# Kernel tuning notes

Hardware: AMD Instinct MI355X
Metric: run time of the kernel (lower is better)

The kernel has to match this reference:

```python
import jax, jax.numpy as jnp
import numpy as np

H, B, T = 4, 16, 4000
E, D, A, C, K, O = 512, 512, 128, 10, 101, 512


def setup_inputs() -> dict:
    key = jax.random.key(0)
    ks = jax.random.split(key, 12)
    return {
        "enc_pad": jax.random.normal(ks[0], (B, T, E), jnp.float32),
        "enc_len": jax.random.randint(ks[1], (B,), T // 2, T + 1, jnp.int32),
        "dec_z": jax.random.normal(ks[2], (B, D), jnp.float32),
        "att_prev": jax.random.uniform(ks[3], (H, B, T), jnp.float32) / T,
        # learned parameters (per-head stacks)
        "Wenc": jax.random.normal(ks[4], (H, E, A), jnp.float32) / np.sqrt(E).astype(np.float32),
        "benc": jnp.zeros((H, A), jnp.float32),
        "Wdec": jax.random.normal(ks[5], (H, D, A), jnp.float32) / np.sqrt(D).astype(np.float32),
        "Watt": jax.random.normal(ks[6], (H, C, A), jnp.float32) / np.sqrt(C).astype(np.float32),
        "conv_w": jax.random.normal(ks[7], (H, C, K), jnp.float32) / np.sqrt(K).astype(np.float32),
        "gv": jax.random.normal(ks[8], (H, A), jnp.float32) / np.sqrt(A).astype(np.float32),
        "Wo": jax.random.normal(ks[9], (H * E, O), jnp.float32) / np.sqrt(H * E).astype(np.float32),
        "bo": jnp.zeros((O,), jnp.float32),
    }


def reference(enc_pad, enc_len, dec_z, att_prev, Wenc, benc, Wdec, Watt, conv_w, gv, Wo, bo):
    scaling = 1.0
    Hh, Bb, Tt = att_prev.shape
    Cc, Kk = conv_w.shape[1], conv_w.shape[2]
    pad_l = Kk // 2
    pad_r = Kk // 2 if Kk % 2 == 1 else Kk // 2 - 1
    # location conv: grouped 1D conv over heads. lhs [B,H,Tp], rhs [H*C,1,K]
    x = jnp.pad(att_prev.transpose(1, 0, 2), ((0, 0), (0, 0), (pad_l, pad_r)))
    rhs = conv_w.reshape(Hh * Cc, 1, Kk)
    conv = jax.lax.conv_general_dilated(
        x, rhs, window_strides=(1,), padding='VALID',
        dimension_numbers=('NCH', 'OIH', 'NCH'), feature_group_count=Hh)  # [B,H*C,T]
    conv = conv.reshape(Bb, Hh, Cc, Tt)
    att_conv = jnp.einsum('bhct,hca->bhta', conv, Watt)                    # mlp_att
    enc_proj = jnp.einsum('bte,hea->bhta', enc_pad, Wenc) + benc[None, :, None, :]  # mlp_enc
    dec_proj = jnp.einsum('bd,hda->bha', dec_z, Wdec)[:, :, None, :]       # mlp_dec
    e = jnp.einsum('bhta,ha->bht', jnp.tanh(enc_proj + dec_proj + att_conv), gv)  # gvec
    w = jax.nn.softmax(scaling * e, axis=-1)                               # [B,H,T]
    c = jnp.einsum('bht,bte->bhe', w, enc_pad).reshape(Bb, Hh * enc_pad.shape[-1])
    out = c @ Wo + bo                                                      # mlp_o
    return out, w.transpose(1, 0, 2)  # ws stacked as [H,B,T]
```

## Files before the change

### kernel.cpp

```cpp
#include <hip/hip_runtime.h>
#include <hip/hip_bf16.h>

#define H_ 4
#define B_ 16
#define T_ 4000
#define E_ 512
#define D_ 512
#define A_ 128
#define C_ 10
#define K_ 101
#define O_ 512
#define TC_ 50
#define CH_ (T_ / TC_)

typedef __attribute__((ext_vector_type(4))) float f32x4;
typedef __attribute__((ext_vector_type(8)))  short short8;

#define MFMA16(a, b, c) __builtin_amdgcn_mfma_f32_16x16x32_bf16(a, b, c, 0, 0, 0)

#define GLL16(gp, lp) __builtin_amdgcn_global_load_lds( \
    (const __attribute__((address_space(1))) unsigned int*)(gp), \
    (__attribute__((address_space(3))) unsigned int*)(lp), 16, 0, 0)

static __device__ __forceinline__ unsigned short f2bf(float x) {
  unsigned u = __float_as_uint(x);
  unsigned r = (u + 0x7FFFu + ((u >> 16) & 1u)) >> 16;
  return (unsigned short)r;
}
static __device__ __forceinline__ unsigned pk2(float a, float b) {
  return (unsigned)f2bf(a) | ((unsigned)f2bf(b) << 16);
}
static __device__ __forceinline__ unsigned cvtpk(float lo, float hi) {
  unsigned r;
  asm("v_cvt_pk_bf16_f32 %0, %1, %2" : "=v"(r) : "v"(lo), "v"(hi));
  return r;
}
static __device__ __forceinline__ uint4 packbf8(float4 f0, float4 f1) {
  uint4 u;
  u.x = cvtpk(f0.x, f0.y); u.y = cvtpk(f0.z, f0.w);
  u.z = cvtpk(f1.x, f1.y); u.w = cvtpk(f1.z, f1.w);
  return u;
}
static __device__ __forceinline__ float tanh_fast(float x) {
  return 1.0f - 2.0f / (__expf(2.0f * x) + 1.0f);
}
static __device__ __forceinline__ int swz(int r) {
  return (r & 3) ^ ((r >> 2) & 3);
}

__global__ __launch_bounds__(256) void k_prep(const float* __restrict__ Wenc,
                                              const float* __restrict__ Watt,
                                              const float* __restrict__ dec_z,
                                              const float* __restrict__ Wdec,
                                              const float* __restrict__ benc,
                                              char* __restrict__ wbs2,
                                              char* __restrict__ wattb2,
                                              float* __restrict__ addv4) {
  const int bid = blockIdx.x;
  const int tid = threadIdx.x;
  if (bid < 128) {
    const int c = bid * 256 + tid;
    const int kt = c >> 11;
    const int ci = c & 2047;
    const int col = ci >> 2, cc = ci & 3;
    const int h = col >> 7, a = col & 127;
    const int kk = kt * 32 + ((cc ^ swz(col)) & 3) * 8;
    const float* w = Wenc + ((size_t)h * E_ + kk) * A_ + a;
    uint4 u;
    u.x = pk2(w[0], w[A_]);
    u.y = pk2(w[2 * A_], w[3 * A_]);
    u.z = pk2(w[4 * A_], w[5 * A_]);
    u.w = pk2(w[6 * A_], w[7 * A_]);
    ((uint4*)wbs2)[c] = u;
  } else if (bid == 128) {
#pragma unroll
    for (int q = 0; q < 4; ++q) {
      const int cw = q * 256 + tid;
      const int h = cw >> 8;
      const int rr = cw & 255;
      const int col = rr >> 1, half = rr & 1;
      unsigned short v[8];
#pragma unroll
      for (int j = 0; j < 8; ++j) {
        const int k = half * 8 + j;
        v[j] = (k < C_) ? f2bf(Watt[((size_t)h * C_ + k) * A_ + col]) : (unsigned short)0;
      }
      uint4 u;
      u.x = (unsigned)v[0] | ((unsigned)v[1] << 16);
      u.y = (unsigned)v[2] | ((unsigned)v[3] << 16);
      u.z = (unsigned)v[4] | ((unsigned)v[5] << 16);
      u.w = (unsigned)v[6] | ((unsigned)v[7] << 16);
      ((uint4*)wattb2)[cw] = u;
    }
  } else {
    const int idx = bid - 129;
    const int b = idx >> 3, h = (idx >> 1) & 3, ks = idx & 1;
    const int a = tid & 127, kh = tid >> 7;
    const int p = ks * 2 + kh;
    const int d0 = p * 128;
    const float* z = dec_z + (size_t)b * D_ + d0;
    const float* w = Wdec + ((size_t)h * D_ + d0) * A_ + a;
    float s = (p == 0) ? benc[h * A_ + a] : 0.f;
#pragma unroll 8
    for (int d = 0; d < 128; ++d) s += z[d] * w[(size_t)d * A_];
    addv4[(((size_t)p * B_ + b) * H_ + h) * A_ + a] = s;
  }
}

__global__ __launch_bounds__(256) void k_conv(const float* __restrict__ att_prev,
                                              const float* __restrict__ conv_w,
                                              char* __restrict__ convpad) {
  const int bh = blockIdx.x;
  const int b = bh / H_, h = bh % H_;
  const int t0 = blockIdx.y * 256;
  __shared__ float ap[256 + K_ - 1 + 3];
  __shared__ float cw[C_ * K_];
  const float* src = att_prev + ((size_t)h * B_ + b) * T_;
  for (int i = threadIdx.x; i < 256 + K_ - 1; i += 256) {
    int tt = t0 - (K_ / 2) + i;
    ap[i] = (tt >= 0 && tt < T_) ? src[tt] : 0.f;
  }
  for (int i = threadIdx.x; i < C_ * K_; i += 256) cw[i] = conv_w[(size_t)h * C_ * K_ + i];
  __syncthreads();
  const int t = t0 + threadIdx.x;
  if (t < T_) {
    float s[C_];
#pragma unroll
    for (int c = 0; c < C_; ++c) s[c] = 0.f;
    for (int k = 0; k < K_; ++k) {
      float apv = ap[threadIdx.x + k];
#pragma unroll
      for (int c = 0; c < C_; ++c) s[c] += cw[c * K_ + k] * apv;
    }
    uint4 u0, u1;
    u0.x = pk2(s[0], s[1]); u0.y = pk2(s[2], s[3]);
    u0.z = pk2(s[4], s[5]); u0.w = pk2(s[6], s[7]);
    u1.x = pk2(s[8], s[9]); u1.y = 0u; u1.z = 0u; u1.w = 0u;
    char* dst = convpad + (size_t)(b * T_ + t) * 128 + h * 32;
    *(uint4*)dst = u0;
    *(uint4*)(dst + 16) = u1;
  }
}

__global__ __launch_bounds__(512, 4) void k_fused_e_mfma(
    const float* __restrict__ enc,
    const char*  __restrict__ wbs2,
    const char*  __restrict__ convpad,
    const char*  __restrict__ wattb2,
    const float* __restrict__ addv4,
    const float* __restrict__ gv,
    float* __restrict__ e_out) {
  __shared__ char smem[73728];
  const int tid = threadIdx.x;
  const int wv = tid >> 6;
  const int lane = tid & 63, l15 = lane & 15, lg = lane >> 4;
  const int m0 = blockIdx.x * 64;
  const int h = wv >> 1;
  const bool aRole = (wv < 4);

  f32x4 acc[4][4];
#pragma unroll
  for (int i = 0; i < 4; ++i)
#pragma unroll
    for (int j = 0; j < 4; ++j) acc[i][j] = (f32x4){0.f, 0.f, 0.f, 0.f};

  int aOff[4], bOff[4];
#pragma unroll
  for (int q = 0; q < 4; ++q) {
    const int row = q * 16 + l15;
    aOff[q] = row * 64 + (((lg ^ swz(row)) & 3) << 4);
    const int col = wv * 64 + q * 16 + l15;
    bOff[q] = col * 64 + (((lg ^ swz(col)) & 3) << 4);
  }

  const int arow = tid >> 2, ac = tid & 3;
  const int ks = ((ac ^ swz(arow)) & 3) * 8;
  const float* eR = enc + (size_t)(m0 + arow) * E_ + ks;
  const int wOff = arow * 64 + ac * 16;
  const char* bsrc = wbs2 + (size_t)(wv - 4) * 8192 + lane * 16;
  char* bdstBase = smem + 8192 + (wv - 4) * 8192;

  float4 X0, X1;
  const float* eP = eR + 64;
  const char* bsP = bsrc + 32768;

  if (aRole) {
    float4 c0 = *(const float4*)eR;
    float4 c1 = *(const float4*)(eR + 4);
    X0 = *(const float4*)(eR + 32);
    X1 = *(const float4*)(eR + 36);
    *(uint4*)(smem + wOff) = packbf8(c0, c1);
    asm volatile("s_waitcnt vmcnt(2) lgkmcnt(0)" ::: "memory");
  } else {
#pragma unroll
    for (int i = 0; i < 8; ++i)
      GLL16(bsrc + i * 1024, bdstBase + i * 1024);
    asm volatile("s_waitcnt vmcnt(0) lgkmcnt(0)" ::: "memory");
  }
  __builtin_amdgcn_sched_barrier(0);
  __builtin_amdgcn_s_barrier();

#pragma unroll 1
  for (int kt = 0; kt < 16; ++kt) {
    const int cur = kt & 1;
    const char* bufA = smem + cur * 4096;
    const char* bufB = smem + 8192 + cur * 32768;

    if (!aRole && kt < 15) {
      char* d = smem + 8192 + (cur ^ 1) * 32768 + (wv - 4) * 8192;
#pragma unroll
      for (int i = 0; i < 8; ++i)
        GLL16(bsP + i * 1024, d + i * 1024);
    }
    __builtin_amdgcn_sched_barrier(0);

    short8 aF[4];
#pragma unroll
    for (int q = 0; q < 4; ++q) aF[q] = *(const short8*)(bufA + aOff[q]);
    __builtin_amdgcn_s_setprio(1);
#pragma unroll
    for (int qn = 0; qn < 4; ++qn) {
      short8 bF = *(const short8*)(bufB + bOff[qn]);
#pragma unroll
      for (int qm = 0; qm < 4; ++qm)
        acc[qm][qn] = MFMA16(aF[qm], bF, acc[qm][qn]);
    }
    __builtin_amdgcn_s_setprio(0);

    if (aRole) {
      if (kt < 15)
        *(uint4*)(smem + (cur ^ 1) * 4096 + wOff) = packbf8(X0, X1);
      if (kt < 14) {
        X0 = *(const float4*)eP;
        X1 = *(const float4*)(eP + 4);
        eP += 32;
      }
    } else {
      bsP += 32768;
    }

    if (kt < 14) {
      if (aRole)
        asm volatile("s_waitcnt vmcnt(2) lgkmcnt(0)" ::: "memory");
      else
        asm volatile("s_waitcnt vmcnt(0) lgkmcnt(0)" ::: "memory");
    } else {
      asm volatile("s_waitcnt vmcnt(0) lgkmcnt(0)" ::: "memory");
    }
    __builtin_amdgcn_sched_barrier(0);
    __builtin_amdgcn_s_barrier();
  }

  {
    short8 zf;
#pragma unroll
    for (int i = 0; i < 8; ++i) zf[i] = 0;
    short8 cf[4], wf[4];
#pragma unroll
    for (int q = 0; q < 4; ++q) { cf[q] = zf; wf[q] = zf; }
    if (lg < 2) {
#pragma unroll
      for (int q = 0; q < 4; ++q) {
        const int row = m0 + q * 16 + l15;
        cf[q] = *(const short8*)(convpad + (size_t)row * 128 + h * 32 + lg * 16);
        const int col = (wv & 1) * 64 + q * 16 + l15;
        wf[q] = *(const short8*)(wattb2 + ((size_t)h * 128 + col) * 32 + lg * 16);
      }
    }
#pragma unroll
    for (int qm = 0; qm < 4; ++qm)
#pragma unroll
      for (int qn = 0; qn < 4; ++qn)
        acc[qm][qn] = MFMA16(cf[qm], wf[qn], acc[qm][qn]);
  }

  {
    const unsigned b0w = (unsigned)m0 / 4000u;
    const unsigned b1w = (unsigned)(m0 + 63) / 4000u;
    float av0[4], av1[4], gvr[4];
#pragma unroll
    for (int qn = 0; qn < 4; ++qn) {
      const int col = (wv & 1) * 64 + qn * 16 + l15;
      const int i0 = (int)b0w * 512 + h * 128 + col;
      const int i1 = (int)b1w * 512 + h * 128 + col;
      av0[qn] = addv4[i0] + addv4[8192 + i0] + addv4[16384 + i0] + addv4[24576 + i0];
      av1[qn] = addv4[i1] + addv4[8192 + i1] + addv4[16384 + i1] + addv4[24576 + i1];
      gvr[qn] = gv[h * 128 + col];
    }
    float* Pb = (float*)smem;
#pragma unroll
    for (int qm = 0; qm < 4; ++qm) {
#pragma unroll
      for (int r = 0; r < 4; ++r) {
        const int rowLocal = qm * 16 + lg * 4 + r;
        const unsigned brow = (unsigned)(m0 + rowLocal);
        const unsigned bb = brow / 4000u;
        const int sel = (bb != b0w);
        float s = 0.f;
#pragma unroll
        for (int qn = 0; qn < 4; ++qn)
          s += gvr[qn] * tanh_fast(acc[qm][qn][r] + (sel ? av1[qn] : av0[qn]));
        s += __shfl_xor(s, 1);
        s += __shfl_xor(s, 2);
        s += __shfl_xor(s, 4);
        s += __shfl_xor(s, 8);
        if (l15 == 0) Pb[wv * 64 + rowLocal] = s;
      }
    }
  }
  __syncthreads();
  if (tid < 256) {
    const float* Pb = (const float*)smem;
    const int hh = tid >> 6, r = tid & 63;
    const float ev = Pb[(hh * 2) * 64 + r] + Pb[(hh * 2 + 1) * 64 + r];
    const unsigned brow = (unsigned)(m0 + r);
    const unsigned bb = brow / 4000u;
    const unsigned tt = brow - bb * 4000u;
    e_out[((size_t)bb * H_ + hh) * T_ + tt] = ev;
  }
}

__global__ __launch_bounds__(256) void k_msum(const float* __restrict__ e_in,
                                              float2* __restrict__ msum) {
  const int bh = blockIdx.x;
  const float* er = e_in + (size_t)bh * T_;
  __shared__ float red[256];
  const int tid = threadIdx.x;
  float m = -1e30f;
  for (int t = tid; t < T_; t += 256) m = fmaxf(m, er[t]);
  red[tid] = m;
  __syncthreads();
  for (int s = 128; s > 0; s >>= 1) {
    if (tid < s) red[tid] = fmaxf(red[tid], red[tid + s]);
    __syncthreads();
  }
  m = red[0];
  __syncthreads();
  float sum = 0.f;
  for (int t = tid; t < T_; t += 256) sum += __expf(er[t] - m);
  red[tid] = sum;
  __syncthreads();
  for (int s = 128; s > 0; s >>= 1) {
    if (tid < s) red[tid] += red[tid + s];
    __syncthreads();
  }
  if (tid == 0) msum[bh] = make_float2(m, 1.0f / red[0]);
}

__global__ __launch_bounds__(512) void k_ctx(const float* __restrict__ enc,
                                             const float* __restrict__ e_in,
                                             const float2* __restrict__ msum,
                                             float* __restrict__ wout,
                                             float* __restrict__ partial) {
  const int b = blockIdx.x, tc = blockIdx.y;
  const int t0 = tc * CH_;
  const int tid = threadIdx.x;
  const int grp = tid >> 7, lt = tid & 127;
  __shared__ float wls[H_ * CH_];
  __shared__ float4 red[3][4][128];
  for (int i = tid; i < H_ * CH_; i += 512) {
    const int h = i / CH_, tt = i - h * CH_;
    const float2 ms = msum[b * H_ + h];
    const float w = __expf(e_in[((size_t)b * H_ + h) * T_ + t0 + tt] - ms.x) * ms.y;
    wls[i] = w;
    wout[((size_t)h * B_ + b) * T_ + t0 + tt] = w;
  }
  __syncthreads();
  float4 a0 = {0,0,0,0}, a1 = {0,0,0,0}, a2 = {0,0,0,0}, a3 = {0,0,0,0};
  const float4* enc4 = (const float4*)enc;
  const int tg = grp * 20;
  const size_t ebase = ((size_t)b * T_ + t0 + tg) * 128 + lt;
#pragma unroll 5
  for (int tt = 0; tt < 20; ++tt) {
    const float4 x = enc4[ebase + (size_t)tt * 128];
    const float w0 = wls[tg + tt];
    const float w1 = wls[CH_ + tg + tt];
    const float w2 = wls[2 * CH_ + tg + tt];
    const float w3 = wls[3 * CH_ + tg + tt];
    a0.x += w0 * x.x; a0.y += w0 * x.y; a0.z += w0 * x.z; a0.w += w0 * x.w;
    a1.x += w1 * x.x; a1.y += w1 * x.y; a1.z += w1 * x.z; a1.w += w1 * x.w;
    a2.x += w2 * x.x; a2.y += w2 * x.y; a2.z += w2 * x.z; a2.w += w2 * x.w;
    a3.x += w3 * x.x; a3.y += w3 * x.y; a3.z += w3 * x.z; a3.w += w3 * x.w;
  }
  if (grp > 0) {
    red[grp - 1][0][lt] = a0;
    red[grp - 1][1][lt] = a1;
    red[grp - 1][2][lt] = a2;
    red[grp - 1][3][lt] = a3;
  }
  __syncthreads();
  if (grp == 0) {
#pragma unroll
    for (int g = 0; g < 3; ++g) {
      const float4 r0 = red[g][0][lt], r1 = red[g][1][lt];
      const float4 r2 = red[g][2][lt], r3 = red[g][3][lt];
      a0.x += r0.x; a0.y += r0.y; a0.z += r0.z; a0.w += r0.w;
      a1.x += r1.x; a1.y += r1.y; a1.z += r1.z; a1.w += r1.w;
      a2.x += r2.x; a2.y += r2.y; a2.z += r2.z; a2.w += r2.w;
      a3.x += r3.x; a3.y += r3.y; a3.z += r3.z; a3.w += r3.w;
    }
    float4* p4 = (float4*)partial;
    const size_t pbase = (((size_t)tc * B_ + b) * H_) * 128 + lt;
    p4[pbase] = a0;
    p4[pbase + 128] = a1;
    p4[pbase + 256] = a2;
    p4[pbase + 384] = a3;
  }
}

__global__ __launch_bounds__(256) void k_out_part(const float* __restrict__ partial,
                                                  const float* __restrict__ Wo,
                                                  float* __restrict__ p2) {
  const int b = blockIdx.x;
  const int o = blockIdx.y * 256 + threadIdx.x;
  const int kc = blockIdx.z;
  __shared__ float cS[256];
  const int he0 = kc * 256;
  {
    float s = 0.f;
#pragma unroll
    for (int tc = 0; tc < TC_; ++tc)
      s += partial[((size_t)tc * B_ + b) * (H_ * E_) + he0 + threadIdx.x];
    cS[threadIdx.x] = s;
  }
  __syncthreads();
  float s = 0.f;
#pragma unroll 8
  for (int i = 0; i < 256; ++i) s += cS[i] * Wo[(size_t)(he0 + i) * O_ + o];
  p2[((size_t)kc * B_ + b) * O_ + o] = s;
}

__global__ __launch_bounds__(512) void k_out_fin(const float* __restrict__ p2,
                                                 const float* __restrict__ bo,
                                                 float* __restrict__ out) {
  const int b = blockIdx.x, o = threadIdx.x;
  float s = bo[o];
#pragma unroll
  for (int kc = 0; kc < 8; ++kc) s += p2[((size_t)kc * B_ + b) * O_ + o];
  out[b * O_ + o] = s;
}

extern "C" void kernel_launch(void* const* d_in, const int* in_sizes, int n_in,
                              void* d_out, int out_size, void* d_ws, size_t ws_size,
                              hipStream_t stream) {
  (void)in_sizes; (void)n_in; (void)out_size; (void)ws_size;
  const float* enc      = (const float*)d_in[0];
  const float* dec_z    = (const float*)d_in[2];
  const float* att_prev = (const float*)d_in[3];
  const float* Wenc     = (const float*)d_in[4];
  const float* benc     = (const float*)d_in[5];
  const float* Wdec     = (const float*)d_in[6];
  const float* Watt     = (const float*)d_in[7];
  const float* conv_w   = (const float*)d_in[8];
  const float* gv       = (const float*)d_in[9];
  const float* Wo       = (const float*)d_in[10];
  const float* bo       = (const float*)d_in[11];

  float* out  = (float*)d_out;
  float* wout = out + B_ * O_;

  char* wsb = (char*)d_ws;
  float*  e_buf   = (float*)(wsb);
  char*   convpad = wsb + 1024000;
  char*   wbs2    = wsb + 9216000;
  char*   wattb2  = wsb + 9740288;
  float*  addv4   = (float*)(wsb + 9756672);
  float2* msum    = (float2*)(wsb + 9887744);
  float*  partial = (float*)(wsb + 9888256);
  float*  p2      = (float*)(wsb + 16441856);

  hipLaunchKernelGGL(k_prep, dim3(257), dim3(256), 0, stream,
                     Wenc, Watt, dec_z, Wdec, benc, wbs2, wattb2, addv4);
  hipLaunchKernelGGL(k_conv, dim3(B_ * H_, 16), dim3(256), 0, stream, att_prev, conv_w, convpad);
  hipLaunchKernelGGL(k_fused_e_mfma, dim3(1000), dim3(512), 0, stream,
                     enc, wbs2, convpad, wattb2, addv4, gv, e_buf);
  hipLaunchKernelGGL(k_msum, dim3(B_ * H_), dim3(256), 0, stream, e_buf, msum);
  hipLaunchKernelGGL(k_ctx, dim3(B_, TC_), dim3(512), 0, stream, enc, e_buf, msum, wout, partial);
  hipLaunchKernelGGL(k_out_part, dim3(B_, O_ / 256, 8), dim3(256), 0, stream, partial, Wo, p2);
  hipLaunchKernelGGL(k_out_fin, dim3(B_), dim3(512), 0, stream, p2, bo, out);
}
```

Before: 143.4 us.

## Fuse conv into prep kernel and replace softmax max pass with gv-norm bound

Merges the location-conv kernel into the prep kernel as extra blocks, removing one launch. It also drops the separate max/sum softmax kernel. The fixed shift is now sum|gv| per head, which bounds e because |tanh|<=1. The exp-sums are accumulated with atomics in the score kernel's epilogue. This saves a launch and a full pass over e, in exchange for atomic contention and float-order nondeterminism. The shift relies on the bound to avoid overflow and could lose precision if it is far above the real max.

```diff
diff --git a/kernel.cpp b/kernel.cpp
--- a/kernel.cpp
+++ b/kernel.cpp
@@ -48,17 +48,49 @@
   return (r & 3) ^ ((r >> 2) & 3);
 }
 
-__global__ __launch_bounds__(256) void k_prep(const float* __restrict__ Wenc,
-                                              const float* __restrict__ Watt,
-                                              const float* __restrict__ dec_z,
-                                              const float* __restrict__ Wdec,
-                                              const float* __restrict__ benc,
-                                              char* __restrict__ wbs2,
-                                              char* __restrict__ wattb2,
-                                              float* __restrict__ addv4) {
+__global__ __launch_bounds__(256) void k_prepconv(
+    const float* __restrict__ Wenc, const float* __restrict__ Watt,
+    const float* __restrict__ dec_z, const float* __restrict__ Wdec,
+    const float* __restrict__ benc, const float* __restrict__ att_prev,
+    const float* __restrict__ conv_w, const float* __restrict__ gv,
+    char* __restrict__ wbs2, char* __restrict__ wattb2,
+    float* __restrict__ addv4, char* __restrict__ convpad,
+    float* __restrict__ msM, float* __restrict__ sums) {
+  __shared__ float ap[256 + K_ - 1 + 3];
+  __shared__ float cw[C_ * K_];
   const int bid = blockIdx.x;
   const int tid = threadIdx.x;
-  if (bid < 128) {
+  if (bid >= 257) {
+    const int cid = bid - 257;
+    const int bh = cid & 63;
+    const int b = bh / H_, h = bh % H_;
+    const int t0 = (cid >> 6) * 256;
+    const float* src = att_prev + ((size_t)h * B_ + b) * T_;
+    for (int i = tid; i < 256 + K_ - 1; i += 256) {
+      int tt = t0 - (K_ / 2) + i;
+      ap[i] = (tt >= 0 && tt < T_) ? src[tt] : 0.f;
+    }
+    for (int i = tid; i < C_ * K_; i += 256) cw[i] = conv_w[(size_t)h * C_ * K_ + i];
+    __syncthreads();
+    const int t = t0 + tid;
+    if (t < T_) {
+      float s[C_];
+#pragma unroll
+      for (int c = 0; c < C_; ++c) s[c] = 0.f;
+      for (int k = 0; k < K_; ++k) {
+        float apv = ap[tid + k];
+#pragma unroll
+        for (int c = 0; c < C_; ++c) s[c] += cw[c * K_ + k] * apv;
+      }
+      uint4 u0, u1;
+      u0.x = pk2(s[0], s[1]); u0.y = pk2(s[2], s[3]);
+      u0.z = pk2(s[4], s[5]); u0.w = pk2(s[6], s[7]);
+      u1.x = pk2(s[8], s[9]); u1.y = 0u; u1.z = 0u; u1.w = 0u;
+      char* dst = convpad + (size_t)(b * T_ + t) * 128 + h * 32;
+      *(uint4*)dst = u0;
+      *(uint4*)(dst + 16) = u1;
+    }
+  } else if (bid < 128) {
     const int c = bid * 256 + tid;
     const int kt = c >> 11;
     const int ci = c & 2047;
@@ -75,9 +107,9 @@
   } else if (bid == 128) {
 #pragma unroll
     for (int q = 0; q < 4; ++q) {
-      const int cw = q * 256 + tid;
-      const int h = cw >> 8;
-      const int rr = cw & 255;
+      const int cw2 = q * 256 + tid;
+      const int h = cw2 >> 8;
+      const int rr = cw2 & 255;
       const int col = rr >> 1, half = rr & 1;
       unsigned short v[8];
 #pragma unroll
@@ -90,8 +122,15 @@
       u.y = (unsigned)v[2] | ((unsigned)v[3] << 16);
       u.z = (unsigned)v[4] | ((unsigned)v[5] << 16);
       u.w = (unsigned)v[6] | ((unsigned)v[7] << 16);
-      ((uint4*)wattb2)[cw] = u;
-    }
+      ((uint4*)wattb2)[cw2] = u;
+    }
+    if (tid < 4) {
+      float m = 0.f;
+#pragma unroll 8
+      for (int a = 0; a < A_; ++a) m += fabsf(gv[tid * A_ + a]);
+      msM[tid] = m;
+    }
+    if (tid >= 4 && tid < 68) sums[tid - 4] = 0.f;
   } else {
     const int idx = bid - 129;
     const int b = idx >> 3, h = (idx >> 1) & 3, ks = idx & 1;
@@ -107,41 +146,6 @@
   }
 }
 
-__global__ __launch_bounds__(256) void k_conv(const float* __restrict__ att_prev,
-                                              const float* __restrict__ conv_w,
-                                              char* __restrict__ convpad) {
-  const int bh = blockIdx.x;
-  const int b = bh / H_, h = bh % H_;
-  const int t0 = blockIdx.y * 256;
-  __shared__ float ap[256 + K_ - 1 + 3];
-  __shared__ float cw[C_ * K_];
-  const float* src = att_prev + ((size_t)h * B_ + b) * T_;
-  for (int i = threadIdx.x; i < 256 + K_ - 1; i += 256) {
-    int tt = t0 - (K_ / 2) + i;
-    ap[i] = (tt >= 0 && tt < T_) ? src[tt] : 0.f;
-  }
-  for (int i = threadIdx.x; i < C_ * K_; i += 256) cw[i] = conv_w[(size_t)h * C_ * K_ + i];
-  __syncthreads();
-  const int t = t0 + threadIdx.x;
-  if (t < T_) {
-    float s[C_];
-#pragma unroll
-    for (int c = 0; c < C_; ++c) s[c] = 0.f;
-    for (int k = 0; k < K_; ++k) {
-      float apv = ap[threadIdx.x + k];
-#pragma unroll
-      for (int c = 0; c < C_; ++c) s[c] += cw[c * K_ + k] * apv;
-    }
-    uint4 u0, u1;
-    u0.x = pk2(s[0], s[1]); u0.y = pk2(s[2], s[3]);
-    u0.z = pk2(s[4], s[5]); u0.w = pk2(s[6], s[7]);
-    u1.x = pk2(s[8], s[9]); u1.y = 0u; u1.z = 0u; u1.w = 0u;
-    char* dst = convpad + (size_t)(b * T_ + t) * 128 + h * 32;
-    *(uint4*)dst = u0;
-    *(uint4*)(dst + 16) = u1;
-  }
-}
-
 __global__ __launch_bounds__(512, 4) void k_fused_e_mfma(
     const float* __restrict__ enc,
     const char*  __restrict__ wbs2,
@@ -149,6 +153,8 @@
     const char*  __restrict__ wattb2,
     const float* __restrict__ addv4,
     const float* __restrict__ gv,
+    const float* __restrict__ msM,
+    float* __restrict__ sums,
     float* __restrict__ e_out) {
   __shared__ char smem[73728];
   const int tid = threadIdx.x;
@@ -317,39 +323,28 @@
     const unsigned bb = brow / 4000u;
     const unsigned tt = brow - bb * 4000u;
     e_out[((size_t)bb * H_ + hh) * T_ + tt] = ev;
-  }
-}
-
-__global__ __launch_bounds__(256) void k_msum(const float* __restrict__ e_in,
-                                              float2* __restrict__ msum) {
-  const int bh = blockIdx.x;
-  const float* er = e_in + (size_t)bh * T_;
-  __shared__ float red[256];
-  const int tid = threadIdx.x;
-  float m = -1e30f;
-  for (int t = tid; t < T_; t += 256) m = fmaxf(m, er[t]);
-  red[tid] = m;
-  __syncthreads();
-  for (int s = 128; s > 0; s >>= 1) {
-    if (tid < s) red[tid] = fmaxf(red[tid], red[tid + s]);
-    __syncthreads();
-  }
-  m = red[0];
-  __syncthreads();
-  float sum = 0.f;
-  for (int t = tid; t < T_; t += 256) sum += __expf(er[t] - m);
-  red[tid] = sum;
-  __syncthreads();
-  for (int s = 128; s > 0; s >>= 1) {
-    if (tid < s) red[tid] += red[tid + s];
-    __syncthreads();
-  }
-  if (tid == 0) msum[bh] = make_float2(m, 1.0f / red[0]);
+    const float x = __expf(ev - msM[hh]);
+    const unsigned b0w = (unsigned)m0 / 4000u;
+    float x0 = (bb == b0w) ? x : 0.f;
+    float x1 = (bb == b0w) ? 0.f : x;
+    x0 += __shfl_xor(x0, 1);  x1 += __shfl_xor(x1, 1);
+    x0 += __shfl_xor(x0, 2);  x1 += __shfl_xor(x1, 2);
+    x0 += __shfl_xor(x0, 4);  x1 += __shfl_xor(x1, 4);
+    x0 += __shfl_xor(x0, 8);  x1 += __shfl_xor(x1, 8);
+    x0 += __shfl_xor(x0, 16); x1 += __shfl_xor(x1, 16);
+    x0 += __shfl_xor(x0, 32); x1 += __shfl_xor(x1, 32);
+    if ((tid & 63) == 0) {
+      atomicAdd(&sums[b0w * H_ + hh], x0);
+      const unsigned b1w = (unsigned)(m0 + 63) / 4000u;
+      if (b1w != b0w) atomicAdd(&sums[b1w * H_ + hh], x1);
+    }
+  }
 }
 
 __global__ __launch_bounds__(512) void k_ctx(const float* __restrict__ enc,
                                              const float* __restrict__ e_in,
-                                             const float2* __restrict__ msum,
+                                             const float* __restrict__ msM,
+                                             const float* __restrict__ sums,
                                              float* __restrict__ wout,
                                              float* __restrict__ partial) {
   const int b = blockIdx.x, tc = blockIdx.y;
@@ -360,8 +355,8 @@
   __shared__ float4 red[3][4][128];
   for (int i = tid; i < H_ * CH_; i += 512) {
     const int h = i / CH_, tt = i - h * CH_;
-    const float2 ms = msum[b * H_ + h];
-    const float w = __expf(e_in[((size_t)b * H_ + h) * T_ + t0 + tt] - ms.x) * ms.y;
+    const float w = __expf(e_in[((size_t)b * H_ + h) * T_ + t0 + tt] - msM[h]) /
+                    sums[b * H_ + h];
     wls[i] = w;
     wout[((size_t)h * B_ + b) * T_ + t0 + tt] = w;
   }
@@ -465,17 +460,18 @@
   char*   wbs2    = wsb + 9216000;
   char*   wattb2  = wsb + 9740288;
   float*  addv4   = (float*)(wsb + 9756672);
-  float2* msum    = (float2*)(wsb + 9887744);
+  float*  msM     = (float*)(wsb + 9887744);
+  float*  sums    = (float*)(wsb + 9887808);
   float*  partial = (float*)(wsb + 9888256);
   float*  p2      = (float*)(wsb + 16441856);
 
-  hipLaunchKernelGGL(k_prep, dim3(257), dim3(256), 0, stream,
-                     Wenc, Watt, dec_z, Wdec, benc, wbs2, wattb2, addv4);
-  hipLaunchKernelGGL(k_conv, dim3(B_ * H_, 16), dim3(256), 0, stream, att_prev, conv_w, convpad);
+  hipLaunchKernelGGL(k_prepconv, dim3(1281), dim3(256), 0, stream,
+                     Wenc, Watt, dec_z, Wdec, benc, att_prev, conv_w, gv,
+                     wbs2, wattb2, addv4, convpad, msM, sums);
   hipLaunchKernelGGL(k_fused_e_mfma, dim3(1000), dim3(512), 0, stream,
-                     enc, wbs2, convpad, wattb2, addv4, gv, e_buf);
-  hipLaunchKernelGGL(k_msum, dim3(B_ * H_), dim3(256), 0, stream, e_buf, msum);
-  hipLaunchKernelGGL(k_ctx, dim3(B_, TC_), dim3(512), 0, stream, enc, e_buf, msum, wout, partial);
+                     enc, wbs2, convpad, wattb2, addv4, gv, msM, sums, e_buf);
+  hipLaunchKernelGGL(k_ctx, dim3(B_, TC_), dim3(512), 0, stream,
+                     enc, e_buf, msM, sums, wout, partial);
   hipLaunchKernelGGL(k_out_part, dim3(B_, O_ / 256, 8), dim3(256), 0, stream, partial, Wo, p2);
   hipLaunchKernelGGL(k_out_fin, dim3(B_), dim3(512), 0, stream, p2, bo, out);
 }
```

Result: slower. 149.7 us (+4.4%).
